# Kernel tuning notes

Measured on AMD Instinct MI355X. Metric: run time of the kernel, lower is better.

## Reference

```python
import jax, jax.numpy as jnp
import numpy as np

N_NODES = 100000
N_EDGES = 1600000
D = 128


def sage_conv(x, src, dst, W_l, b_l, W_r):
    # mean aggregation of neighbor features: messages flow src -> dst
    msgs = x[src]                                           # [E, D] gather
    agg = jax.ops.segment_sum(msgs, dst, num_segments=x.shape[0])  # [N, D]
    deg = jax.ops.segment_sum(jnp.ones((src.shape[0],), x.dtype), dst,
                              num_segments=x.shape[0])       # [N]
    agg = agg / jnp.maximum(deg, 1.0)[:, None]
    # PyG SAGEConv: lin_l(aggregated) + lin_r(root); bias lives in lin_l
    return agg @ W_l.T + b_l + x @ W_r.T


def setup_inputs() -> dict:
    key = jax.random.key(0)
    ks = jax.random.split(key, 8)
    s = 1.0 / np.sqrt(D)
    return {
        "x": jax.random.normal(ks[0], (N_NODES, D), dtype=jnp.float32),
        "edge_index": jax.random.randint(ks[1], (2, N_EDGES), 0, N_NODES, dtype=jnp.int64),
        "W1_l": jax.random.normal(ks[2], (D, D), dtype=jnp.float32) * s,
        "b1": jnp.zeros((D,), dtype=jnp.float32),
        "W1_r": jax.random.normal(ks[3], (D, D), dtype=jnp.float32) * s,
        "W2_l": jax.random.normal(ks[4], (D, D), dtype=jnp.float32) * s,
        "b2": jnp.zeros((D,), dtype=jnp.float32),
        "W2_r": jax.random.normal(ks[5], (D, D), dtype=jnp.float32) * s,
    }


def reference(x, edge_index, W1_l, b1, W1_r, W2_l, b2, W2_r):
    src, dst = edge_index[0], edge_index[1]
    h = jax.nn.relu(sage_conv(x, src, dst, W1_l, b1, W1_r))
    out = sage_conv(h, src, dst, W2_l, b2, W2_r)
    return out
```

## Files before the change

### kernel.cpp

```cpp
#include <hip/hip_runtime.h>
#include <cstdint>
#include <cstddef>

#define D 128

typedef unsigned short ushort_t;
typedef unsigned int uint_t;
typedef __attribute__((ext_vector_type(8))) short bf16x8;
typedef __attribute__((ext_vector_type(4))) float f32x4;

static __device__ __forceinline__ unsigned short f2bf(float f) {
    unsigned int u = __float_as_uint(f);
    u = (u + 0x7FFFu + ((u >> 16) & 1u)) >> 16;
    return (unsigned short)u;
}
static __device__ __forceinline__ float bf_lo(uint_t v) {
    return __uint_as_float(v << 16);
}
static __device__ __forceinline__ float bf_hi(uint_t v) {
    return __uint_as_float(v & 0xFFFF0000u);
}


__global__ __launch_bounds__(256) void bkt_hist(const int* __restrict__ dst,
                                                int* __restrict__ bhist, int E) {
    __shared__ int lh[512];
    int t = threadIdx.x;
    lh[t] = 0;
    lh[t + 256] = 0;
    __syncthreads();
    int base = blockIdx.x * 4096;
#pragma unroll
    for (int i = 0; i < 16; ++i) {
        int e = base + i * 256 + t;
        if (e < E) atomicAdd(&lh[dst[e] >> 8], 1);
    }
    __syncthreads();
    if (lh[t]) atomicAdd(&bhist[t], lh[t]);
    if (lh[t + 256]) atomicAdd(&bhist[t + 256], lh[t + 256]);
}

__global__ __launch_bounds__(512) void bkt_scan(const int* __restrict__ bhist,
                                                int* __restrict__ boff,
                                                int* __restrict__ bcur,
                                                int* __restrict__ row_ptr,
                                                int N, int E) {
    __shared__ int s[512];
    int t = threadIdx.x;
    int v = bhist[t];
    s[t] = v;
    __syncthreads();
    for (int off = 1; off < 512; off <<= 1) {
        int u = (t >= off) ? s[t - off] : 0;
        __syncthreads();
        s[t] += u;
        __syncthreads();
    }
    int ex = s[t] - v;
    boff[t] = ex;
    bcur[t] = ex;
    if (t == 511) boff[512] = s[511];
    if (t == 0) row_ptr[N] = E;
}

__global__ __launch_bounds__(256) void bkt_scatter(const int* __restrict__ src,
                                                   const int* __restrict__ dst,
                                                   int* __restrict__ bcur,
                                                   int* __restrict__ ebuf, int E) {
    __shared__ int lh[512];
    __shared__ int gb[512];
    int t = threadIdx.x;
    lh[t] = 0;
    lh[t + 256] = 0;
    __syncthreads();
    int base = blockIdx.x * 4096;
    unsigned pk[16];
#pragma unroll
    for (int i = 0; i < 16; ++i) {
        int e = base + i * 256 + t;
        unsigned p = 0xFFFFFFFFu;
        if (e < E) {
            int d = dst[e];
            int bkt = d >> 8;
            int r = atomicAdd(&lh[bkt], 1);
            p = ((unsigned)r << 17) | ((unsigned)bkt << 8) | (unsigned)(d & 255);
        }
        pk[i] = p;
    }
    __syncthreads();
    if (lh[t]) gb[t] = atomicAdd(&bcur[t], lh[t]);
    if (lh[t + 256]) gb[t + 256] = atomicAdd(&bcur[t + 256], lh[t + 256]);
    __syncthreads();
#pragma unroll
    for (int i = 0; i < 16; ++i) {
        int e = base + i * 256 + t;
        if (e < E) {
            unsigned p = pk[i];
            int bkt = (p >> 8) & 511;
            int r = (int)(p >> 17);
            ebuf[gb[bkt] + r] = src[e] | ((int)(p & 255) << 20);
        }
    }
}

__global__ __launch_bounds__(256) void bkt_build(const int* __restrict__ ebuf,
                                                 const int* __restrict__ boff,
                                                 int* __restrict__ row_ptr,
                                                 int* __restrict__ csr, int N) {
    __shared__ int lcnt[256];
    __shared__ int lofs[256];
    __shared__ int lcur[256];
    int t = threadIdx.x;
    int b = blockIdx.x;
    int base = b << 8;
    int ebeg = boff[b], eend = boff[b + 1];
    lcnt[t] = 0;
    __syncthreads();
    for (int e = ebeg + t; e < eend; e += 256)
        atomicAdd(&lcnt[((unsigned)ebuf[e]) >> 20], 1);
    __syncthreads();
    int v = lcnt[t];
    lofs[t] = v;
    __syncthreads();
    for (int off = 1; off < 256; off <<= 1) {
        int u = (t >= off) ? lofs[t - off] : 0;
        __syncthreads();
        lofs[t] += u;
        __syncthreads();
    }
    int ex = lofs[t] - v;
    __syncthreads();
    lofs[t] = ex;
    lcur[t] = 0;
    if (base + t < N) row_ptr[base + t] = ebeg + ex;
    __syncthreads();
    for (int e = ebeg + t; e < eend; e += 256) {
        int u = ebuf[e];
        int d = ((unsigned)u) >> 20;
        int r = atomicAdd(&lcur[d], 1);
        csr[ebeg + lofs[d] + r] = u & 0xFFFFF;
    }
}


__global__ __launch_bounds__(256) void cast_x_kernel(const float* __restrict__ src,
                                                     ushort_t* __restrict__ dst,
                                                     long n) {
    long i = ((long)blockIdx.x * 256 + threadIdx.x) * 8;
    if (i >= n) return;
    float4 a = *(const float4*)(src + i);
    float4 b = *(const float4*)(src + i + 4);
    uint4 o;
    o.x = (uint_t)f2bf(a.x) | ((uint_t)f2bf(a.y) << 16);
    o.y = (uint_t)f2bf(a.z) | ((uint_t)f2bf(a.w) << 16);
    o.z = (uint_t)f2bf(b.x) | ((uint_t)f2bf(b.y) << 16);
    o.w = (uint_t)f2bf(b.z) | ((uint_t)f2bf(b.w) << 16);
    *(uint4*)(dst + i) = o;
}

__global__ __launch_bounds__(256) void cast_w_kernel(const float* __restrict__ s0,
                                                     const float* __restrict__ s1,
                                                     const float* __restrict__ s2,
                                                     const float* __restrict__ s3,
                                                     ushort_t* __restrict__ d0,
                                                     ushort_t* __restrict__ d1,
                                                     ushort_t* __restrict__ d2,
                                                     ushort_t* __restrict__ d3) {
    const float* s = (blockIdx.y == 0) ? s0 : (blockIdx.y == 1) ? s1
                   : (blockIdx.y == 2) ? s2 : s3;
    ushort_t* d = (blockIdx.y == 0) ? d0 : (blockIdx.y == 1) ? d1
                : (blockIdx.y == 2) ? d2 : d3;
    long i = ((long)blockIdx.x * 256 + threadIdx.x) * 8;
    float4 a = *(const float4*)(s + i);
    float4 b = *(const float4*)(s + i + 4);
    uint4 o;
    o.x = (uint_t)f2bf(a.x) | ((uint_t)f2bf(a.y) << 16);
    o.y = (uint_t)f2bf(a.z) | ((uint_t)f2bf(a.w) << 16);
    o.z = (uint_t)f2bf(b.x) | ((uint_t)f2bf(b.y) << 16);
    o.w = (uint_t)f2bf(b.z) | ((uint_t)f2bf(b.w) << 16);
    *(uint4*)(d + i) = o;
}


static __device__ __forceinline__ void acc8(uint4 v, float a[8]) {
    a[0] += bf_lo(v.x); a[1] += bf_hi(v.x);
    a[2] += bf_lo(v.y); a[3] += bf_hi(v.y);
    a[4] += bf_lo(v.z); a[5] += bf_hi(v.z);
    a[6] += bf_lo(v.w); a[7] += bf_hi(v.w);
}

static __device__ __forceinline__ uint4 grow(const ushort_t* __restrict__ xin,
                                             int s, int l16) {
    unsigned off = ((unsigned)s << 8) | ((unsigned)l16 << 4);
    return *(const uint4*)((const char*)xin + off);
}

__global__ __launch_bounds__(256) void agg_b_kernel(const ushort_t* __restrict__ xin,
                                                    const int* __restrict__ csr,
                                                    const int* __restrict__ row_ptr,
                                                    ushort_t* __restrict__ aggb, int N) {
    int node = blockIdx.x * 4 + (threadIdx.x >> 6);
    if (node >= N) return;
    int lane = threadIdx.x & 63;
    int g = lane >> 4;
    int l16 = lane & 15;
    int beg = row_ptr[node], end = row_ptr[node + 1];
    int deg = end - beg;
    float a[8] = {0.f, 0.f, 0.f, 0.f, 0.f, 0.f, 0.f, 0.f};

    if (deg > 0) {
        int deg64 = min(deg, 64);
        int ld = csr[beg + min(lane, deg - 1)];
        int myidx = (lane < deg64) ? ld : 0x7FFFFFFF;
#pragma unroll
        for (int k = 2; k <= 64; k <<= 1) {
#pragma unroll
            for (int j = k >> 1; j > 0; j >>= 1) {
                int o = __shfl_xor(myidx, j);
                bool lower = (lane & j) == 0;
                bool asc = (lane & k) == 0;
                myidx = (lower == asc) ? min(myidx, o) : max(myidx, o);
            }
        }
        int e = 0;
        for (; e + 16 <= deg64; e += 16) {
            int s0 = __shfl(myidx, e + g);
            int s1 = __shfl(myidx, e + 4 + g);
            int s2 = __shfl(myidx, e + 8 + g);
            int s3 = __shfl(myidx, e + 12 + g);
            uint4 v0 = grow(xin, s0, l16);
            uint4 v1 = grow(xin, s1, l16);
            uint4 v2 = grow(xin, s2, l16);
            uint4 v3 = grow(xin, s3, l16);
            acc8(v0, a); acc8(v1, a); acc8(v2, a); acc8(v3, a);
        }
        if (e + 8 <= deg64) {
            int s0 = __shfl(myidx, e + g);
            int s1 = __shfl(myidx, e + 4 + g);
            uint4 v0 = grow(xin, s0, l16);
            uint4 v1 = grow(xin, s1, l16);
            acc8(v0, a); acc8(v1, a);
            e += 8;
        }
        if (e + 4 <= deg64) {
            int s0 = __shfl(myidx, e + g);
            uint4 v0 = grow(xin, s0, l16);
            acc8(v0, a);
            e += 4;
        }
        if (e < deg64) {
            int ee = min(e + g, deg64 - 1);
            int s = __shfl(myidx, ee);
            uint4 v = grow(xin, s, l16);
            if (e + g < deg64) acc8(v, a);
        }
        for (int e2 = 64; e2 < deg; e2 += 4) {
            int s = csr[beg + min(e2 + g, deg - 1)];
            uint4 v = grow(xin, s, l16);
            if (e2 + g < deg) acc8(v, a);
        }
    }

#pragma unroll
    for (int i = 0; i < 8; ++i) {
        a[i] += __shfl_xor(a[i], 16);
        a[i] += __shfl_xor(a[i], 32);
    }
    if (g == 0) {
        float inv = 1.0f / fmaxf((float)deg, 1.0f);
        uint4 o;
        o.x = (uint_t)f2bf(a[0] * inv) | ((uint_t)f2bf(a[1] * inv) << 16);
        o.y = (uint_t)f2bf(a[2] * inv) | ((uint_t)f2bf(a[3] * inv) << 16);
        o.z = (uint_t)f2bf(a[4] * inv) | ((uint_t)f2bf(a[5] * inv) << 16);
        o.w = (uint_t)f2bf(a[6] * inv) | ((uint_t)f2bf(a[7] * inv) << 16);
        unsigned off = ((unsigned)node << 8) | ((unsigned)l16 << 4);
        *(uint4*)((char*)aggb + off) = o;
    }
}


__global__ __launch_bounds__(256) void gemm_mfma(const ushort_t* __restrict__ Aagg,
                                                 const ushort_t* __restrict__ Ax,
                                                 const ushort_t* __restrict__ Wl,
                                                 const ushort_t* __restrict__ Wr,
                                                 const float* __restrict__ bias,
                                                 ushort_t* __restrict__ out_bf,
                                                 float* __restrict__ out_f32,
                                                 int N, int relu_bf) {
    __shared__ ushort_t sA[128 * 32];
    __shared__ ushort_t sW[128 * 32];
    int tid = threadIdx.x;
    int wave = tid >> 6, lane = tid & 63;
    int quad = lane >> 4, l15 = lane & 15;
    int wm = wave & 1, wc = wave >> 1;
    int n0 = blockIdx.x * 128;

    int sr = tid >> 2;
    int sseg = (tid & 3) * 8;

    f32x4 acc[4][4];
#pragma unroll
    for (int mt = 0; mt < 4; ++mt)
#pragma unroll
        for (int nt = 0; nt < 4; ++nt) acc[mt][nt] = (f32x4){0.f, 0.f, 0.f, 0.f};

    int ga0 = min(n0 + sr, N - 1);
    int ga1 = min(n0 + sr + 64, N - 1);

#pragma unroll
    for (int c = 0; c < 8; ++c) {
        const ushort_t* Ab = (c < 4) ? Aagg : Ax;
        const ushort_t* Wb = (c < 4) ? Wl : Wr;
        int koff = (c & 3) * 32 + sseg;
        bf16x8 va0 = *(const bf16x8*)(Ab + (size_t)ga0 * D + koff);
        bf16x8 va1 = *(const bf16x8*)(Ab + (size_t)ga1 * D + koff);
        bf16x8 vw0 = *(const bf16x8*)(Wb + (size_t)sr * D + koff);
        bf16x8 vw1 = *(const bf16x8*)(Wb + (size_t)(sr + 64) * D + koff);
        __syncthreads();
        *(bf16x8*)&sA[sr * 32 + sseg] = va0;
        *(bf16x8*)&sA[(sr + 64) * 32 + sseg] = va1;
        *(bf16x8*)&sW[sr * 32 + sseg] = vw0;
        *(bf16x8*)&sW[(sr + 64) * 32 + sseg] = vw1;
        __syncthreads();

        bf16x8 af[4], wf[4];
#pragma unroll
        for (int mt = 0; mt < 4; ++mt)
            af[mt] = *(const bf16x8*)&sA[(wm * 64 + mt * 16 + l15) * 32 + quad * 8];
#pragma unroll
        for (int nt = 0; nt < 4; ++nt)
            wf[nt] = *(const bf16x8*)&sW[(wc * 64 + nt * 16 + l15) * 32 + quad * 8];
#pragma unroll
        for (int mt = 0; mt < 4; ++mt)
#pragma unroll
            for (int nt = 0; nt < 4; ++nt)
                acc[mt][nt] = __builtin_amdgcn_mfma_f32_16x16x32_bf16(
                    af[mt], wf[nt], acc[mt][nt], 0, 0, 0);
    }

#pragma unroll
    for (int mt = 0; mt < 4; ++mt) {
#pragma unroll
        for (int nt = 0; nt < 4; ++nt) {
            int col = wc * 64 + nt * 16 + l15;
            float bv = bias[col];
#pragma unroll
            for (int reg = 0; reg < 4; ++reg) {
                int row = n0 + wm * 64 + mt * 16 + quad * 4 + reg;
                if (row < N) {
                    float v = acc[mt][nt][reg] + bv;
                    if (relu_bf) {
                        v = fmaxf(v, 0.f);
                        out_bf[(size_t)row * D + col] = f2bf(v);
                    } else {
                        out_f32[(size_t)row * D + col] = v;
                    }
                }
            }
        }
    }
}


extern "C" void kernel_launch(void* const* d_in, const int* in_sizes, int n_in,
                              void* d_out, int out_size, void* d_ws, size_t ws_size,
                              hipStream_t stream) {
    const float* x   = (const float*)d_in[0];
    const int*   ei  = (const int*)d_in[1];
    const float* W1l = (const float*)d_in[2];
    const float* b1  = (const float*)d_in[3];
    const float* W1r = (const float*)d_in[4];
    const float* W2l = (const float*)d_in[5];
    const float* b2  = (const float*)d_in[6];
    const float* W2r = (const float*)d_in[7];
    float* out = (float*)d_out;

    int N = in_sizes[0] / D;
    int E = in_sizes[1] / 2;
    const int* src = ei;
    const int* dst = ei + E;

    char* ws = (char*)d_ws;
    size_t off = 0;
    auto take = [&](size_t bytes) -> char* {
        char* p = ws + off;
        off += (bytes + 255) & ~(size_t)255;
        return p;
    };
    int*      row_ptr = (int*)take((size_t)(N + 1) * sizeof(int));
    int*      bhist   = (int*)take((size_t)(512 + 512 + 513) * sizeof(int));
    int*      bcur    = bhist + 512;
    int*      boff    = bhist + 1024;
    int*      ebuf    = (int*)take((size_t)E * sizeof(int));
    int*      csr     = (int*)take((size_t)E * sizeof(int));
    ushort_t* xb      = (ushort_t*)take((size_t)N * D * sizeof(ushort_t));
    ushort_t* hb      = (ushort_t*)take((size_t)N * D * sizeof(ushort_t));
    ushort_t* aggb    = (ushort_t*)take((size_t)N * D * sizeof(ushort_t));
    ushort_t* W1lb    = (ushort_t*)take((size_t)D * D * sizeof(ushort_t));
    ushort_t* W1rb    = (ushort_t*)take((size_t)D * D * sizeof(ushort_t));
    ushort_t* W2lb    = (ushort_t*)take((size_t)D * D * sizeof(ushort_t));
    ushort_t* W2rb    = (ushort_t*)take((size_t)D * D * sizeof(ushort_t));
    (void)ws_size;
    (void)n_in;
    (void)out_size;

    hipMemsetAsync(bhist, 0, 1024 * sizeof(int), stream);

    int NB = (N + 255) / 256;
    int EB = (E + 4095) / 4096;

    bkt_hist<<<EB, 256, 0, stream>>>(dst, bhist, E);
    bkt_scan<<<1, 512, 0, stream>>>(bhist, boff, bcur, row_ptr, N, E);
    bkt_scatter<<<EB, 256, 0, stream>>>(src, dst, bcur, ebuf, E);
    bkt_build<<<NB, 256, 0, stream>>>(ebuf, boff, row_ptr, csr, N);

    long nx = (long)N * D;
    cast_x_kernel<<<(int)((nx / 8 + 255) / 256), 256, 0, stream>>>(x, xb, nx);
    cast_w_kernel<<<dim3(8, 4), 256, 0, stream>>>(W1l, W1r, W2l, W2r,
                                                  W1lb, W1rb, W2lb, W2rb);

    int ablocks = (N + 3) / 4;
    int gblocks = (N + 127) / 128;

    agg_b_kernel<<<ablocks, 256, 0, stream>>>(xb, csr, row_ptr, aggb, N);
    gemm_mfma<<<gblocks, 256, 0, stream>>>(aggb, xb, W1lb, W1rb, b1, hb, nullptr, N, 1);

    agg_b_kernel<<<ablocks, 256, 0, stream>>>(hb, csr, row_ptr, aggb, N);
    gemm_mfma<<<gblocks, 256, 0, stream>>>(aggb, hb, W2lb, W2rb, b2, nullptr, out, N, 0);
}
```

Baseline: 366.8 us.

## Fuse whole two-layer pipeline into one cooperative persistent megakernel

```diff
diff --git a/kernel.cpp b/kernel.cpp
--- a/kernel.cpp
+++ b/kernel.cpp
@@ -1,8 +1,11 @@
 #include <hip/hip_runtime.h>
+#include <hip/hip_cooperative_groups.h>
 #include <cstdint>
 #include <cstddef>
 
 #define D 128
+
+namespace cg = cooperative_groups;
 
 typedef unsigned short ushort_t;
 typedef unsigned int uint_t;
@@ -19,6 +22,352 @@
 }
 static __device__ __forceinline__ float bf_hi(uint_t v) {
     return __uint_as_float(v & 0xFFFF0000u);
+}
+
+static __device__ __forceinline__ void cast8(const float* __restrict__ s,
+                                             ushort_t* __restrict__ d) {
+    float4 a = *(const float4*)s;
+    float4 b = *(const float4*)(s + 4);
+    uint4 o;
+    o.x = (uint_t)f2bf(a.x) | ((uint_t)f2bf(a.y) << 16);
+    o.y = (uint_t)f2bf(a.z) | ((uint_t)f2bf(a.w) << 16);
+    o.z = (uint_t)f2bf(b.x) | ((uint_t)f2bf(b.y) << 16);
+    o.w = (uint_t)f2bf(b.z) | ((uint_t)f2bf(b.w) << 16);
+    *(uint4*)d = o;
+}
+
+static __device__ __forceinline__ void acc8(uint4 v, float a[8]) {
+    a[0] += bf_lo(v.x); a[1] += bf_hi(v.x);
+    a[2] += bf_lo(v.y); a[3] += bf_hi(v.y);
+    a[4] += bf_lo(v.z); a[5] += bf_hi(v.z);
+    a[6] += bf_lo(v.w); a[7] += bf_hi(v.w);
+}
+
+static __device__ __forceinline__ uint4 grow(const ushort_t* __restrict__ xin,
+                                             int s, int l16) {
+    unsigned off = ((unsigned)s << 8) | ((unsigned)l16 << 4);
+    return *(const uint4*)((const char*)xin + off);
+}
+
+
+struct MegaP {
+    const float* x;
+    const int* src;
+    const int* dst;
+    const float* W1l; const float* b1; const float* W1r;
+    const float* W2l; const float* b2; const float* W2r;
+    float* out;
+    int* row_ptr; int* bhist; int* bcur; int* boff;
+    int* ebuf; int* csr;
+    ushort_t* xb; ushort_t* hb;
+    ushort_t* W1lb; ushort_t* W1rb; ushort_t* W2lb; ushort_t* W2rb;
+    int N, E, EB, NB, NT;
+};
+
+#define AGG_STRIDE_B 272
+
+static __device__ __forceinline__ void layer_fused(
+    const ushort_t* __restrict__ xin, const int* __restrict__ csr,
+    const int* __restrict__ row_ptr, const ushort_t* __restrict__ Wl,
+    const ushort_t* __restrict__ Wr, const float* __restrict__ bias,
+    ushort_t* __restrict__ out_bf, float* __restrict__ out_f32,
+    int N, int relu_bf, int NT,
+    char* sac, ushort_t* sW, ushort_t* sX) {
+    int tid = threadIdx.x;
+    int wave = tid >> 6, lane = tid & 63;
+    int g = lane >> 4, l16 = lane & 15;
+    int quad = lane >> 4, l15 = lane & 15;
+    int wm = wave & 1, wc = wave >> 1;
+    int sr = tid >> 2;
+    int sseg = (tid & 3) * 8;
+
+    for (int tile = blockIdx.x; tile < NT; tile += gridDim.x) {
+        __syncthreads();
+        int n0 = tile * 128;
+
+        for (int i = 0; i < 32; i += 2) {
+            int r0 = wave * 32 + i, r1 = r0 + 1;
+            int node0 = min(n0 + r0, N - 1);
+            int node1 = min(n0 + r1, N - 1);
+            int b0 = row_ptr[node0];
+            int deg0 = row_ptr[node0 + 1] - b0;
+            int b1 = row_ptr[node1];
+            int deg1 = row_ptr[node1 + 1] - b1;
+            int d0 = min(deg0, 64), d1 = min(deg1, 64);
+            int i0 = (deg0 > 0) ? csr[b0 + min(lane, deg0 - 1)] : 0;
+            int i1 = (deg1 > 0) ? csr[b1 + min(lane, deg1 - 1)] : 0;
+            int c0 = (d0 > 0 ? d0 : 1) - 1;
+            int c1 = (d1 > 0 ? d1 : 1) - 1;
+            float a0[8] = {0.f, 0.f, 0.f, 0.f, 0.f, 0.f, 0.f, 0.f};
+            float a1[8] = {0.f, 0.f, 0.f, 0.f, 0.f, 0.f, 0.f, 0.f};
+            int mm = max(d0, d1);
+            for (int e = 0; e < mm; e += 16) {
+                uint4 v0[4], v1[4];
+#pragma unroll
+                for (int q = 0; q < 4; ++q) {
+                    int s = __shfl(i0, min(e + 4 * q + g, c0));
+                    v0[q] = grow(xin, s, l16);
+                }
+#pragma unroll
+                for (int q = 0; q < 4; ++q) {
+                    int s = __shfl(i1, min(e + 4 * q + g, c1));
+                    v1[q] = grow(xin, s, l16);
+                }
+#pragma unroll
+                for (int q = 0; q < 4; ++q)
+                    if (e + 4 * q + g < d0) acc8(v0[q], a0);
+#pragma unroll
+                for (int q = 0; q < 4; ++q)
+                    if (e + 4 * q + g < d1) acc8(v1[q], a1);
+            }
+            for (int e2 = 64; e2 < deg0; e2 += 4) {
+                int s = csr[b0 + min(e2 + g, deg0 - 1)];
+                uint4 v = grow(xin, s, l16);
+                if (e2 + g < deg0) acc8(v, a0);
+            }
+            for (int e2 = 64; e2 < deg1; e2 += 4) {
+                int s = csr[b1 + min(e2 + g, deg1 - 1)];
+                uint4 v = grow(xin, s, l16);
+                if (e2 + g < deg1) acc8(v, a1);
+            }
+#pragma unroll
+            for (int k = 0; k < 8; ++k) {
+                a0[k] += __shfl_xor(a0[k], 16);
+                a0[k] += __shfl_xor(a0[k], 32);
+                a1[k] += __shfl_xor(a1[k], 16);
+                a1[k] += __shfl_xor(a1[k], 32);
+            }
+            if (g == 0) {
+                float inv0 = 1.0f / fmaxf((float)deg0, 1.0f);
+                uint4 o0;
+                o0.x = (uint_t)f2bf(a0[0] * inv0) | ((uint_t)f2bf(a0[1] * inv0) << 16);
+                o0.y = (uint_t)f2bf(a0[2] * inv0) | ((uint_t)f2bf(a0[3] * inv0) << 16);
+                o0.z = (uint_t)f2bf(a0[4] * inv0) | ((uint_t)f2bf(a0[5] * inv0) << 16);
+                o0.w = (uint_t)f2bf(a0[6] * inv0) | ((uint_t)f2bf(a0[7] * inv0) << 16);
+                *(uint4*)(sac + r0 * AGG_STRIDE_B + l16 * 16) = o0;
+                float inv1 = 1.0f / fmaxf((float)deg1, 1.0f);
+                uint4 o1;
+                o1.x = (uint_t)f2bf(a1[0] * inv1) | ((uint_t)f2bf(a1[1] * inv1) << 16);
+                o1.y = (uint_t)f2bf(a1[2] * inv1) | ((uint_t)f2bf(a1[3] * inv1) << 16);
+                o1.z = (uint_t)f2bf(a1[4] * inv1) | ((uint_t)f2bf(a1[5] * inv1) << 16);
+                o1.w = (uint_t)f2bf(a1[6] * inv1) | ((uint_t)f2bf(a1[7] * inv1) << 16);
+                *(uint4*)(sac + r1 * AGG_STRIDE_B + l16 * 16) = o1;
+            }
+        }
+
+        f32x4 acc[4][4];
+#pragma unroll
+        for (int mt = 0; mt < 4; ++mt)
+#pragma unroll
+            for (int nt = 0; nt < 4; ++nt) acc[mt][nt] = (f32x4){0.f, 0.f, 0.f, 0.f};
+
+        int ga0 = min(n0 + sr, N - 1);
+        int ga1 = min(n0 + sr + 64, N - 1);
+
+#pragma unroll
+        for (int c = 0; c < 8; ++c) {
+            const ushort_t* Wb = (c < 4) ? Wl : Wr;
+            int koff = (c & 3) * 32 + sseg;
+            bf16x8 vw0 = *(const bf16x8*)(Wb + (size_t)sr * D + koff);
+            bf16x8 vw1 = *(const bf16x8*)(Wb + (size_t)(sr + 64) * D + koff);
+            bf16x8 va0, va1;
+            if (c >= 4) {
+                va0 = *(const bf16x8*)(xin + (size_t)ga0 * D + koff);
+                va1 = *(const bf16x8*)(xin + (size_t)ga1 * D + koff);
+            }
+            __syncthreads();
+            *(bf16x8*)&sW[sr * 32 + sseg] = vw0;
+            *(bf16x8*)&sW[(sr + 64) * 32 + sseg] = vw1;
+            if (c >= 4) {
+                *(bf16x8*)&sX[sr * 32 + sseg] = va0;
+                *(bf16x8*)&sX[(sr + 64) * 32 + sseg] = va1;
+            }
+            __syncthreads();
+
+            bf16x8 af[4], wf[4];
+#pragma unroll
+            for (int mt = 0; mt < 4; ++mt) {
+                int row = wm * 64 + mt * 16 + l15;
+                af[mt] = (c < 4)
+                    ? *(const bf16x8*)(sac + row * AGG_STRIDE_B + ((c & 3) * 32 + quad * 8) * 2)
+                    : *(const bf16x8*)&sX[row * 32 + quad * 8];
+            }
+#pragma unroll
+            for (int nt = 0; nt < 4; ++nt)
+                wf[nt] = *(const bf16x8*)&sW[(wc * 64 + nt * 16 + l15) * 32 + quad * 8];
+#pragma unroll
+            for (int mt = 0; mt < 4; ++mt)
+#pragma unroll
+                for (int nt = 0; nt < 4; ++nt)
+                    acc[mt][nt] = __builtin_amdgcn_mfma_f32_16x16x32_bf16(
+                        af[mt], wf[nt], acc[mt][nt], 0, 0, 0);
+        }
+
+#pragma unroll
+        for (int mt = 0; mt < 4; ++mt) {
+#pragma unroll
+            for (int nt = 0; nt < 4; ++nt) {
+                int col = wc * 64 + nt * 16 + l15;
+                float bv = bias[col];
+#pragma unroll
+                for (int reg = 0; reg < 4; ++reg) {
+                    int row = n0 + wm * 64 + mt * 16 + quad * 4 + reg;
+                    if (row < N) {
+                        float v = acc[mt][nt][reg] + bv;
+                        if (relu_bf) {
+                            v = fmaxf(v, 0.f);
+                            out_bf[(size_t)row * D + col] = f2bf(v);
+                        } else {
+                            out_f32[(size_t)row * D + col] = v;
+                        }
+                    }
+                }
+            }
+        }
+    }
+}
+
+__global__ __launch_bounds__(256, 3) void mega(MegaP P) {
+    __shared__ ushort_t sAgg[128 * 136];
+    __shared__ ushort_t sW[128 * 32];
+    __shared__ ushort_t sX[128 * 32];
+    int* si = (int*)sAgg;
+    char* sac = (char*)sAgg;
+    cg::grid_group gg = cg::this_grid();
+    int t = threadIdx.x, bid = blockIdx.x, gsz = gridDim.x;
+    int N = P.N, E = P.E;
+
+    for (int i = bid * 256 + t; i < 1024; i += gsz * 256) P.bhist[i] = 0;
+    gg.sync();
+
+    for (int chunk = bid; chunk < P.EB; chunk += gsz) {
+        si[t] = 0;
+        si[t + 256] = 0;
+        __syncthreads();
+        int base = chunk * 4096;
+#pragma unroll
+        for (int k = 0; k < 16; ++k) {
+            int e = base + k * 256 + t;
+            if (e < E) atomicAdd(&si[P.dst[e] >> 8], 1);
+        }
+        __syncthreads();
+        if (si[t]) atomicAdd(&P.bhist[t], si[t]);
+        if (si[t + 256]) atomicAdd(&P.bhist[t + 256], si[t + 256]);
+        __syncthreads();
+    }
+    {
+        int items = (N * D) >> 3;
+        for (int i = bid * 256 + t; i < items; i += gsz * 256)
+            cast8(P.x + (size_t)i * 8, P.xb + (size_t)i * 8);
+        for (int i = bid * 256 + t; i < 4 * 2048; i += gsz * 256) {
+            int arr = i >> 11;
+            int j = (i & 2047) * 8;
+            const float* s = (arr == 0) ? P.W1l : (arr == 1) ? P.W1r
+                           : (arr == 2) ? P.W2l : P.W2r;
+            ushort_t* d = (arr == 0) ? P.W1lb : (arr == 1) ? P.W1rb
+                        : (arr == 2) ? P.W2lb : P.W2rb;
+            cast8(s + j, d + j);
+        }
+    }
+    gg.sync();
+
+    if (bid == 0) {
+        int a0 = P.bhist[2 * t], a1 = P.bhist[2 * t + 1];
+        int ps = a0 + a1;
+        si[t] = ps;
+        __syncthreads();
+        for (int off = 1; off < 256; off <<= 1) {
+            int u = (t >= off) ? si[t - off] : 0;
+            __syncthreads();
+            si[t] += u;
+            __syncthreads();
+        }
+        int inc = si[t];
+        int exb = inc - ps;
+        P.boff[2 * t] = exb;
+        P.bcur[2 * t] = exb;
+        P.boff[2 * t + 1] = exb + a0;
+        P.bcur[2 * t + 1] = exb + a0;
+        if (t == 255) P.boff[512] = inc;
+        if (t == 0) P.row_ptr[N] = E;
+    }
+    gg.sync();
+
+    for (int chunk = bid; chunk < P.EB; chunk += gsz) {
+        si[t] = 0;
+        si[t + 256] = 0;
+        __syncthreads();
+        int base = chunk * 4096;
+        unsigned pk[16];
+#pragma unroll
+        for (int k = 0; k < 16; ++k) {
+            int e = base + k * 256 + t;
+            unsigned p = 0xFFFFFFFFu;
+            if (e < E) {
+                int d = P.dst[e];
+                int bkt = d >> 8;
+                int r = atomicAdd(&si[bkt], 1);
+                p = ((unsigned)r << 17) | ((unsigned)bkt << 8) | (unsigned)(d & 255);
+            }
+            pk[k] = p;
+        }
+        __syncthreads();
+        if (si[t]) si[512 + t] = atomicAdd(&P.bcur[t], si[t]);
+        if (si[t + 256]) si[512 + t + 256] = atomicAdd(&P.bcur[t + 256], si[t + 256]);
+        __syncthreads();
+#pragma unroll
+        for (int k = 0; k < 16; ++k) {
+            int e = base + k * 256 + t;
+            if (e < E) {
+                unsigned p = pk[k];
+                int bkt = (p >> 8) & 511;
+                int r = (int)(p >> 17);
+                P.ebuf[si[512 + bkt] + r] = P.src[e] | ((int)(p & 255) << 20);
+            }
+        }
+        __syncthreads();
+    }
+    gg.sync();
+
+    for (int b = bid; b < P.NB; b += gsz) {
+        int base = b << 8;
+        int ebeg = P.boff[b], eend = P.boff[b + 1];
+        si[t] = 0;
+        __syncthreads();
+        for (int e = ebeg + t; e < eend; e += 256)
+            atomicAdd(&si[((unsigned)P.ebuf[e]) >> 20], 1);
+        __syncthreads();
+        int v = si[t];
+        si[256 + t] = v;
+        __syncthreads();
+        for (int off = 1; off < 256; off <<= 1) {
+            int u = (t >= off) ? si[256 + t - off] : 0;
+            __syncthreads();
+            si[256 + t] += u;
+            __syncthreads();
+        }
+        int ex = si[256 + t] - v;
+        __syncthreads();
+        si[256 + t] = ex;
+        si[512 + t] = 0;
+        if (base + t < N) P.row_ptr[base + t] = ebeg + ex;
+        __syncthreads();
+        for (int e = ebeg + t; e < eend; e += 256) {
+            int u = P.ebuf[e];
+            int d = ((unsigned)u) >> 20;
+            int r = atomicAdd(&si[512 + d], 1);
+            P.csr[ebeg + si[256 + d] + r] = u & 0xFFFFF;
+        }
+        __syncthreads();
+    }
+    gg.sync();
+
+    layer_fused(P.xb, P.csr, P.row_ptr, P.W1lb, P.W1rb, P.b1,
+                P.hb, nullptr, N, 1, P.NT, sac, sW, sX);
+    gg.sync();
+
+    layer_fused(P.hb, P.csr, P.row_ptr, P.W2lb, P.W2rb, P.b2,
+                nullptr, P.out, N, 0, P.NT, sac, sW, sX);
 }
 
 
@@ -142,20 +491,12 @@
     }
 }
 
-
 __global__ __launch_bounds__(256) void cast_x_kernel(const float* __restrict__ src,
                                                      ushort_t* __restrict__ dst,
                                                      long n) {
     long i = ((long)blockIdx.x * 256 + threadIdx.x) * 8;
     if (i >= n) return;
-    float4 a = *(const float4*)(src + i);
-    float4 b = *(const float4*)(src + i + 4);
-    uint4 o;
-    o.x = (uint_t)f2bf(a.x) | ((uint_t)f2bf(a.y) << 16);
-    o.y = (uint_t)f2bf(a.z) | ((uint_t)f2bf(a.w) << 16);
-    o.z = (uint_t)f2bf(b.x) | ((uint_t)f2bf(b.y) << 16);
-    o.w = (uint_t)f2bf(b.z) | ((uint_t)f2bf(b.w) << 16);
-    *(uint4*)(dst + i) = o;
+    cast8(src + i, dst + i);
 }
 
 __global__ __launch_bounds__(256) void cast_w_kernel(const float* __restrict__ s0,
@@ -171,28 +512,7 @@
     ushort_t* d = (blockIdx.y == 0) ? d0 : (blockIdx.y == 1) ? d1
                 : (blockIdx.y == 2) ? d2 : d3;
     long i = ((long)blockIdx.x * 256 + threadIdx.x) * 8;
-    float4 a = *(const float4*)(s + i);
-    float4 b = *(const float4*)(s + i + 4);
-    uint4 o;
-    o.x = (uint_t)f2bf(a.x) | ((uint_t)f2bf(a.y) << 16);
-    o.y = (uint_t)f2bf(a.z) | ((uint_t)f2bf(a.w) << 16);
-    o.z = (uint_t)f2bf(b.x) | ((uint_t)f2bf(b.y) << 16);
-    o.w = (uint_t)f2bf(b.z) | ((uint_t)f2bf(b.w) << 16);
-    *(uint4*)(d + i) = o;
-}
-
-
-static __device__ __forceinline__ void acc8(uint4 v, float a[8]) {
-    a[0] += bf_lo(v.x); a[1] += bf_hi(v.x);
-    a[2] += bf_lo(v.y); a[3] += bf_hi(v.y);
-    a[4] += bf_lo(v.z); a[5] += bf_hi(v.z);
-    a[6] += bf_lo(v.w); a[7] += bf_hi(v.w);
-}
-
-static __device__ __forceinline__ uint4 grow(const ushort_t* __restrict__ xin,
-                                             int s, int l16) {
-    unsigned off = ((unsigned)s << 8) | ((unsigned)l16 << 4);
-    return *(const uint4*)((const char*)xin + off);
+    cast8(s + i, d + i);
 }
 
 __global__ __launch_bounds__(256) void agg_b_kernel(const ushort_t* __restrict__ xin,
@@ -210,18 +530,7 @@
 
     if (deg > 0) {
         int deg64 = min(deg, 64);
-        int ld = csr[beg + min(lane, deg - 1)];
-        int myidx = (lane < deg64) ? ld : 0x7FFFFFFF;
-#pragma unroll
-        for (int k = 2; k <= 64; k <<= 1) {
-#pragma unroll
-            for (int j = k >> 1; j > 0; j >>= 1) {
-                int o = __shfl_xor(myidx, j);
-                bool lower = (lane & j) == 0;
-                bool asc = (lane & k) == 0;
-                myidx = (lower == asc) ? min(myidx, o) : max(myidx, o);
-            }
-        }
+        int myidx = csr[beg + min(lane, deg - 1)];
         int e = 0;
         for (; e + 16 <= deg64; e += 16) {
             int s0 = __shfl(myidx, e + g);
@@ -277,7 +586,6 @@
         *(uint4*)((char*)aggb + off) = o;
     }
 }
-
 
 __global__ __launch_bounds__(256) void gemm_mfma(const ushort_t* __restrict__ Aagg,
                                                  const ushort_t* __restrict__ Ax,
@@ -294,7 +602,6 @@
     int quad = lane >> 4, l15 = lane & 15;
     int wm = wave & 1, wc = wave >> 1;
     int n0 = blockIdx.x * 128;
-
     int sr = tid >> 2;
     int sseg = (tid & 3) * 8;
 
@@ -404,27 +711,54 @@
     (void)n_in;
     (void)out_size;
 
-    hipMemsetAsync(bhist, 0, 1024 * sizeof(int), stream);
-
-    int NB = (N + 255) / 256;
-    int EB = (E + 4095) / 4096;
-
-    bkt_hist<<<EB, 256, 0, stream>>>(dst, bhist, E);
-    bkt_scan<<<1, 512, 0, stream>>>(bhist, boff, bcur, row_ptr, N, E);
-    bkt_scatter<<<EB, 256, 0, stream>>>(src, dst, bcur, ebuf, E);
-    bkt_build<<<NB, 256, 0, stream>>>(ebuf, boff, row_ptr, csr, N);
-
-    long nx = (long)N * D;
-    cast_x_kernel<<<(int)((nx / 8 + 255) / 256), 256, 0, stream>>>(x, xb, nx);
-    cast_w_kernel<<<dim3(8, 4), 256, 0, stream>>>(W1l, W1r, W2l, W2r,
-                                                  W1lb, W1rb, W2lb, W2rb);
-
-    int ablocks = (N + 3) / 4;
-    int gblocks = (N + 127) / 128;
-
-    agg_b_kernel<<<ablocks, 256, 0, stream>>>(xb, csr, row_ptr, aggb, N);
-    gemm_mfma<<<gblocks, 256, 0, stream>>>(aggb, xb, W1lb, W1rb, b1, hb, nullptr, N, 1);
-
-    agg_b_kernel<<<ablocks, 256, 0, stream>>>(hb, csr, row_ptr, aggb, N);
-    gemm_mfma<<<gblocks, 256, 0, stream>>>(aggb, hb, W2lb, W2rb, b2, nullptr, out, N, 0);
-}
+    MegaP P;
+    P.x = x; P.src = src; P.dst = dst;
+    P.W1l = W1l; P.b1 = b1; P.W1r = W1r;
+    P.W2l = W2l; P.b2 = b2; P.W2r = W2r;
+    P.out = out;
+    P.row_ptr = row_ptr; P.bhist = bhist; P.bcur = bcur; P.boff = boff;
+    P.ebuf = ebuf; P.csr = csr;
+    P.xb = xb; P.hb = hb;
+    P.W1lb = W1lb; P.W1rb = W1rb; P.W2lb = W2lb; P.W2rb = W2rb;
+    P.N = N; P.E = E;
+    P.EB = (E + 4095) / 4096;
+    P.NB = (N + 255) / 256;
+    P.NT = (N + 127) / 128;
+
+    static int s_grid = 0;
+    if (s_grid == 0) {
+        int maxB = 0;
+        hipOccupancyMaxActiveBlocksPerMultiprocessor(&maxB, mega, 256, 0);
+        int dev = 0, numCU = 0;
+        hipGetDevice(&dev);
+        hipDeviceGetAttribute(&numCU, hipDeviceAttributeMultiprocessorCount, dev);
+        if (maxB < 1) maxB = 1;
+        if (numCU < 1) numCU = 256;
+        long g = (long)maxB * numCU;
+        if (g > 2048) g = 2048;
+        s_grid = (int)g;
+    }
+
+    void* kp[] = {(void*)&P};
+    hipError_t err = hipLaunchCooperativeKernel((void*)mega, dim3(s_grid),
+                                                dim3(256), kp, 0, stream);
+    if (err != hipSuccess) {
+        hipMemsetAsync(bhist, 0, 1024 * sizeof(int), stream);
+        int NB = (N + 255) / 256;
+        int EB = (E + 4095) / 4096;
+        bkt_hist<<<EB, 256, 0, stream>>>(dst, bhist, E);
+        bkt_scan<<<1, 512, 0, stream>>>(bhist, boff, bcur, row_ptr, N, E);
+        bkt_scatter<<<EB, 256, 0, stream>>>(src, dst, bcur, ebuf, E);
+        bkt_build<<<NB, 256, 0, stream>>>(ebuf, boff, row_ptr, csr, N);
+        long nx = (long)N * D;
+        cast_x_kernel<<<(int)((nx / 8 + 255) / 256), 256, 0, stream>>>(x, xb, nx);
+        cast_w_kernel<<<dim3(8, 4), 256, 0, stream>>>(W1l, W1r, W2l, W2r,
+                                                      W1lb, W1rb, W2lb, W2rb);
+        int ablocks = (N + 3) / 4;
+        int gblocks = (N + 127) / 128;
+        agg_b_kernel<<<ablocks, 256, 0, stream>>>(xb, csr, row_ptr, aggb, N);
+        gemm_mfma<<<gblocks, 256, 0, stream>>>(aggb, xb, W1lb, W1rb, b1, hb, nullptr, N, 1);
+        agg_b_kernel<<<ablocks, 256, 0, stream>>>(hb, csr, row_ptr, aggb, N);
+        gemm_mfma<<<gblocks, 256, 0, stream>>>(aggb, hb, W2lb, W2rb, b2, nullptr, out, N, 0);
+    }
+}
```

Measured after the change: 770.4 us. +110.1%, slower.
